# Performance work log

Measured on AMD Instinct MI355X. Metric: run time of the kernel, lower is better.

## Reference

```python
import jax, jax.numpy as jnp
import numpy as np

NUM_HEADS = 16
HIDDEN = 1024
HEAD_DIM = HIDDEN // NUM_HEADS
B, S, D = 2, 2048, 1024


def setup_inputs() -> dict:
    key = jax.random.key(0)
    ks = jax.random.split(key, 7)
    scale = 1.0 / np.sqrt(D)
    return {
        "query": jax.random.normal(ks[0], (B, S, D), dtype=jnp.float32),
        "key": jax.random.normal(ks[1], (B, S, D), dtype=jnp.float32),
        "value": jax.random.normal(ks[2], (B, S, D), dtype=jnp.float32),
        "Wk_w": jax.random.normal(ks[3], (HIDDEN, D), dtype=jnp.float32) * scale,
        "Wk_b": jax.random.normal(ks[4], (HIDDEN,), dtype=jnp.float32) * scale,
        "Wv_w": jax.random.normal(ks[5], (HIDDEN, D), dtype=jnp.float32) * scale,
        "Wv_b": jax.random.normal(ks[6], (HIDDEN,), dtype=jnp.float32) * scale,
    }


def reference(query, key, value, Wk_w, Wk_b, Wv_w, Wv_b):
    # NOTE: in the original torch module, self.W_v is assigned twice, so the
    # SAME Linear (Wv) projects both key and value; Wk projects query.
    b, s, _ = query.shape

    def split_heads(x):  # [b,s,hidden] -> [b,h,s,hd]
        return x.reshape(b, s, NUM_HEADS, HEAD_DIM).transpose(0, 2, 1, 3)

    q = split_heads(query @ Wk_w.T + Wk_b)
    k = split_heads(key @ Wv_w.T + Wv_b)
    v = split_heads(value @ Wv_w.T + Wv_b)

    scores = jnp.einsum("bhqd,bhkd->bhqk", q, k) / jnp.sqrt(
        jnp.asarray(HEAD_DIM, dtype=q.dtype))
    probs = jax.nn.softmax(scores, axis=-1)
    out = jnp.einsum("bhqk,bhkd->bhqd", probs, v)
    return out.transpose(0, 2, 1, 3).reshape(b, s, NUM_HEADS * HEAD_DIM)
```

## Files before the change

kernel.cpp:

```cpp
#include <hip/hip_runtime.h>
#include <stdint.h>

typedef unsigned short u16;
typedef uint32_t u32;
typedef __bf16 bf16x8 __attribute__((ext_vector_type(8)));
typedef float f32x4 __attribute__((ext_vector_type(4)));
typedef u16 u16x4 __attribute__((ext_vector_type(4)));
typedef u16 u16x8 __attribute__((ext_vector_type(8)));

#define XQ_OFF 0ul
#define XK_OFF 4194304ul
#define XV_OFF 8388608ul
#define WK_OFF 12582912ul
#define WV_OFF 13631488ul
#define Q_OFF  14680064ul
#define K_OFF  18874368ul
#define V_OFF  23068672ul

#define SCQ 0.18033688011112042f

#if __has_builtin(__builtin_amdgcn_exp2f)
#define EXP2F(x) __builtin_amdgcn_exp2f(x)
#else
#define EXP2F(x) exp2f(x)
#endif

__device__ __forceinline__ u16 f2bf(float f) {
  u32 u = __float_as_uint(f);
  u32 r = (u + 0x7fffu + ((u >> 16) & 1u)) >> 16;
  return (u16)r;
}

__device__ __forceinline__ u32 pk2(float a, float b) {
  typedef __bf16 bf2_t __attribute__((ext_vector_type(2)));
  typedef float f2_t __attribute__((ext_vector_type(2)));
  f2_t v; v[0] = a; v[1] = b;
  bf2_t h = __builtin_convertvector(v, bf2_t);
  union { bf2_t h; u32 u; } cv; cv.h = h; return cv.u;
}

__device__ __forceinline__ void load_lds16(const void* g, void* l) {
  __builtin_amdgcn_global_load_lds(
      (const __attribute__((address_space(1))) u32*)g,
      (__attribute__((address_space(3))) u32*)l, 16, 0, 0);
}

__global__ __launch_bounds__(256) void cvt_tile_kernel(
    const float* __restrict__ xq, const float* __restrict__ xk,
    const float* __restrict__ xv, const float* __restrict__ wk,
    const float* __restrict__ wv, u16* __restrict__ ws) {
  __shared__ u16 tile[4096];
  const int bid = blockIdx.x;
  const float* src; size_t dstbase; int rt, ktp;
  if (bid < 3072) {
    int m = bid >> 10, loc = bid & 1023;
    src = (m == 0) ? xq : (m == 1) ? xk : xv;
    dstbase = (size_t)m * 4194304ul;
    rt = loc >> 4; ktp = loc & 15;
  } else {
    int r2 = bid - 3072;
    int m = r2 >> 8, loc = r2 & 255;
    src = m ? wv : wk;
    dstbase = WK_OFF + (size_t)m * 1048576ul;
    rt = loc >> 4; ktp = loc & 15;
  }
  const int t = threadIdx.x;
  const int row0 = t >> 4, c = t & 15;
  const int k = c * 4;
  const float* s = src + (size_t)(rt * 64 + row0) * 1024ul + ktp * 64 + k;
#pragma unroll
  for (int i = 0; i < 4; ++i) {
    float4 v = *(const float4*)(s + (size_t)i * 16384ul);
    int row = row0 + i * 16;
    u32* p = (u32*)(tile + ((k >> 5) * 2048 + ((k >> 3) & 3) * 512 + row * 8 + (k & 7)));
    p[0] = pk2(v.x, v.y);
    p[1] = pk2(v.z, v.w);
  }
  __syncthreads();
  u16* dst = ws + dstbase + (size_t)(rt * 32 + ktp * 2) * 2048ul;
#pragma unroll
  for (int so = 0; so < 4096; so += 2048)
    *(u16x8*)(dst + so + t * 8) = *(const u16x8*)(tile + so + t * 8);
}

__global__ __launch_bounds__(256) void proj_kernel(u16* __restrict__ ws,
                                                   const float* __restrict__ bk,
                                                   const float* __restrict__ bv) {
  const int proj = blockIdx.z;
  const int mtile = blockIdx.x;
  const int ntile = blockIdx.y;
  const u16* A = ws + (size_t)proj * 4194304ul;
  const u16* Bw = ws + ((proj == 0) ? WK_OFF : WV_OFF);
  const float* bias = (proj == 0) ? bk : bv;
  u16* outQ = ws + Q_OFF;
  u16* outK = ws + K_OFF;
  u16* outV = ws + V_OFF;

  const int t = threadIdx.x;
  const int w = t >> 6, lane = t & 63, g = lane >> 4, c = lane & 15;
  const int wm = w >> 1, wn = w & 1;

  const u16* Aw = A + (size_t)(2 * mtile + wm) * 65536ul + (size_t)g * 512ul + (size_t)c * 8ul;
  const u16* Bb = Bw + (size_t)(2 * ntile + wn) * 65536ul + (size_t)g * 512ul + (size_t)c * 8ul;

  f32x4 acc[4][4];
#pragma unroll
  for (int mt = 0; mt < 4; ++mt)
#pragma unroll
    for (int nt = 0; nt < 4; ++nt) acc[mt][nt] = (f32x4){0.f, 0.f, 0.f, 0.f};

  bf16x8 a0[4], b0[4], a1[4], b1[4];
#pragma unroll
  for (int mt = 0; mt < 4; ++mt) {
    a0[mt] = *(const bf16x8*)(Aw + (size_t)(mt * 16) * 8ul);
    b0[mt] = *(const bf16x8*)(Bb + (size_t)(mt * 16) * 8ul);
  }

#pragma unroll 1
  for (int kk = 0; kk < 32; kk += 2) {
    const u16* An1 = Aw + (size_t)(kk + 1) * 2048ul;
    const u16* Bn1 = Bb + (size_t)(kk + 1) * 2048ul;
#pragma unroll
    for (int mt = 0; mt < 4; ++mt) {
      a1[mt] = *(const bf16x8*)(An1 + (size_t)(mt * 16) * 8ul);
      b1[mt] = *(const bf16x8*)(Bn1 + (size_t)(mt * 16) * 8ul);
    }
#pragma unroll
    for (int mt = 0; mt < 4; ++mt)
#pragma unroll
      for (int nt = 0; nt < 4; ++nt)
        acc[mt][nt] = __builtin_amdgcn_mfma_f32_16x16x32_bf16(a0[mt], b0[nt], acc[mt][nt], 0, 0, 0);
    if (kk + 2 < 32) {
      const u16* An2 = Aw + (size_t)(kk + 2) * 2048ul;
      const u16* Bn2 = Bb + (size_t)(kk + 2) * 2048ul;
#pragma unroll
      for (int mt = 0; mt < 4; ++mt) {
        a0[mt] = *(const bf16x8*)(An2 + (size_t)(mt * 16) * 8ul);
        b0[mt] = *(const bf16x8*)(Bn2 + (size_t)(mt * 16) * 8ul);
      }
    }
#pragma unroll
    for (int mt = 0; mt < 4; ++mt)
#pragma unroll
      for (int nt = 0; nt < 4; ++nt)
        acc[mt][nt] = __builtin_amdgcn_mfma_f32_16x16x32_bf16(a1[mt], b1[nt], acc[mt][nt], 0, 0, 0);
  }

  const int m0 = mtile * 128 + wm * 64, n0 = ntile * 128 + wn * 64;
#pragma unroll
  for (int nt = 0; nt < 4; ++nt) {
    const int col = n0 + nt * 16 + c;
    const float bvv = bias[col];
    const int h = col >> 6, d = col & 63;
#pragma unroll
    for (int mt = 0; mt < 4; ++mt) {
      const int mbase = m0 + mt * 16 + g * 4;
      const int b = mbase >> 11;
      const int bh = b * 16 + h;
      if (proj == 2) {
        const int s = mbase & 2047;
        u16x4 pk;
#pragma unroll
        for (int r = 0; r < 4; ++r) pk[r] = f2bf(acc[mt][nt][r] + bvv);
        size_t idx = (size_t)bh * 131072ul + (size_t)(s >> 6) * 4096ul +
                     (size_t)((s & 63) >> 3) * 512ul + (size_t)d * 8ul + (size_t)(s & 7);
        *(u16x4*)(outV + idx) = pk;
      } else {
        u16* dst = (proj == 0) ? outQ : outK;
#pragma unroll
        for (int r = 0; r < 4; ++r) {
          const int m = mbase + r;
          const int s = m & 2047;
          float y = acc[mt][nt][r] + bvv;
          if (proj == 0) y *= SCQ;
          size_t idx;
          if (proj == 0)
            idx = (size_t)bh * 131072ul + (size_t)(s >> 7) * 8192ul + (size_t)(d >> 3) * 1024ul +
                  (size_t)(s & 127) * 8ul + (size_t)(d & 7);
          else
            idx = (size_t)bh * 131072ul + (size_t)(s >> 6) * 4096ul + (size_t)(d >> 3) * 512ul +
                  (size_t)(s & 63) * 8ul + (size_t)(d & 7);
          dst[idx] = f2bf(y);
        }
      }
    }
  }
}

__global__ __launch_bounds__(256, 2) void attn_kernel(const u16* __restrict__ ws,
                                                      float* __restrict__ out) {
  const int bh = blockIdx.x, qtile = blockIdx.y;
  const int b = bh >> 4, h = bh & 15;
  const int t = threadIdx.x, w = t >> 6, lane = t & 63, g = lane >> 4, c = lane & 15;

  __shared__ u16 Ks[2][4096];
  __shared__ u16 Vs[2][4096];
  __shared__ __align__(16) u16 Ps[4][1280];

  const u16* Qg = ws + Q_OFF + (size_t)bh * 131072ul + (size_t)qtile * 8192ul;
  const u16* Kg = ws + K_OFF + (size_t)bh * 131072ul;
  const u16* Vg = ws + V_OFF + (size_t)bh * 131072ul;

  const int off = t * 16;
  load_lds16((const char*)Kg + off, (char*)Ks[0] + off);
  load_lds16((const char*)Kg + 4096 + off, (char*)Ks[0] + 4096 + off);
  load_lds16((const char*)Vg + off, (char*)Vs[0] + off);
  load_lds16((const char*)Vg + 4096 + off, (char*)Vs[0] + 4096 + off);

  bf16x8 qf[2][2];
#pragma unroll
  for (int ntq = 0; ntq < 2; ++ntq)
#pragma unroll
    for (int ks = 0; ks < 2; ++ks)
      qf[ntq][ks] = *(const bf16x8*)(Qg + (ks * 4 + g) * 1024 + (w * 32 + ntq * 16 + c) * 8);

  u16x8 ou;
#pragma unroll
  for (int i = 0; i < 8; ++i) ou[i] = (u16)0x3F80;
  union { u16x8 u; bf16x8 b; } ocv; ocv.u = ou;
  const bf16x8 onesf = ocv.b;

  f32x4 O[2][4], Lacc[2];
#pragma unroll
  for (int mtq = 0; mtq < 2; ++mtq) {
    Lacc[mtq] = (f32x4){0.f, 0.f, 0.f, 0.f};
#pragma unroll
    for (int nt = 0; nt < 4; ++nt) O[mtq][nt] = (f32x4){0.f, 0.f, 0.f, 0.f};
  }

  u16* Psw = Ps[w];
  __syncthreads();

#pragma unroll 1
  for (int j = 0; j < 32; ++j) {
    const int cur = j & 1;
    if (j < 31) {
      const char* Kn = (const char*)(Kg + (size_t)(j + 1) * 4096ul);
      const char* Vn = (const char*)(Vg + (size_t)(j + 1) * 4096ul);
      char* Kd = (char*)Ks[cur ^ 1];
      char* Vd = (char*)Vs[cur ^ 1];
      load_lds16(Kn + off, Kd + off);
      load_lds16(Kn + 4096 + off, Kd + 4096 + off);
      load_lds16(Vn + off, Vd + off);
      load_lds16(Vn + 4096 + off, Vd + 4096 + off);
    }
    const u16* Kc = Ks[cur];
    const u16* Vc = Vs[cur];

    f32x4 St[4][2];
#pragma unroll
    for (int mtk = 0; mtk < 4; ++mtk)
#pragma unroll
      for (int ntq = 0; ntq < 2; ++ntq) St[mtk][ntq] = (f32x4){0.f, 0.f, 0.f, 0.f};
#pragma unroll
    for (int ks = 0; ks < 2; ++ks) {
      bf16x8 kf[4];
#pragma unroll
      for (int mtk = 0; mtk < 4; ++mtk)
        kf[mtk] = *(const bf16x8*)(Kc + (ks * 4 + g) * 512 + (mtk * 16 + c) * 8);
#pragma unroll
      for (int mtk = 0; mtk < 4; ++mtk)
#pragma unroll
        for (int ntq = 0; ntq < 2; ++ntq)
          St[mtk][ntq] =
              __builtin_amdgcn_mfma_f32_16x16x32_bf16(kf[mtk], qf[ntq][ks], St[mtk][ntq], 0, 0, 0);
    }
#pragma unroll
    for (int mtk = 0; mtk < 4; ++mtk)
#pragma unroll
      for (int ntq = 0; ntq < 2; ++ntq)
#pragma unroll
        for (int r = 0; r < 4; ++r) St[mtk][ntq][r] = EXP2F(St[mtk][ntq][r]);
#pragma unroll
    for (int ksh = 0; ksh < 2; ++ksh) {
#pragma unroll
      for (int ntq = 0; ntq < 2; ++ntq)
#pragma unroll
        for (int m2 = 0; m2 < 2; ++m2) {
          const int mtk = ksh * 2 + m2;
          u32 lo = pk2(St[mtk][ntq][0], St[mtk][ntq][1]);
          u32 hi = pk2(St[mtk][ntq][2], St[mtk][ntq][3]);
          u32* p = (u32*)(Psw + (ntq * 16 + c) * 40 + m2 * 16 + g * 4);
          p[0] = lo; p[1] = hi;
        }
      asm volatile("s_waitcnt lgkmcnt(0)" ::: "memory");
      bf16x8 pf[2], vf[4];
#pragma unroll
      for (int mtq = 0; mtq < 2; ++mtq)
        pf[mtq] = *(const bf16x8*)(Psw + (mtq * 16 + c) * 40 + g * 8);
#pragma unroll
      for (int nt = 0; nt < 4; ++nt)
        vf[nt] = *(const bf16x8*)(Vc + (ksh * 4 + g) * 512 + (nt * 16 + c) * 8);
#pragma unroll
      for (int mtq = 0; mtq < 2; ++mtq) {
        Lacc[mtq] = __builtin_amdgcn_mfma_f32_16x16x32_bf16(pf[mtq], onesf, Lacc[mtq], 0, 0, 0);
#pragma unroll
        for (int nt = 0; nt < 4; ++nt)
          O[mtq][nt] = __builtin_amdgcn_mfma_f32_16x16x32_bf16(pf[mtq], vf[nt], O[mtq][nt], 0, 0, 0);
      }
    }
    __syncthreads();
  }

  const int q0 = qtile * 128 + w * 32;
#pragma unroll
  for (int mtq = 0; mtq < 2; ++mtq)
#pragma unroll
    for (int r = 0; r < 4; ++r) {
      const float inv = 1.0f / Lacc[mtq][r];
      const int q = q0 + mtq * 16 + g * 4 + r;
      float* rowp = out + (size_t)(b * 2048 + q) * 1024ul + h * 64;
#pragma unroll
      for (int nt = 0; nt < 4; ++nt) rowp[nt * 16 + c] = O[mtq][nt][r] * inv;
    }
}

extern "C" void kernel_launch(void* const* d_in, const int* in_sizes, int n_in,
                              void* d_out, int out_size, void* d_ws, size_t ws_size,
                              hipStream_t stream) {
  const float* q = (const float*)d_in[0];
  const float* k = (const float*)d_in[1];
  const float* v = (const float*)d_in[2];
  const float* wk = (const float*)d_in[3];
  const float* bk = (const float*)d_in[4];
  const float* wv = (const float*)d_in[5];
  const float* bv = (const float*)d_in[6];
  u16* ws = (u16*)d_ws;
  float* out = (float*)d_out;

  cvt_tile_kernel<<<3584, 256, 0, stream>>>(q, k, v, wk, wv, ws);
  proj_kernel<<<dim3(32, 8, 3), 256, 0, stream>>>(ws, bk, bv);
  attn_kernel<<<dim3(32, 16), 256, 0, stream>>>(ws, out);
}
```

Measured before the change: 192.8 us.

## Use 32x32 MFMA in projection and double attention waves per block

```diff
diff --git a/kernel.cpp b/kernel.cpp
--- a/kernel.cpp
+++ b/kernel.cpp
@@ -5,6 +5,7 @@
 typedef uint32_t u32;
 typedef __bf16 bf16x8 __attribute__((ext_vector_type(8)));
 typedef float f32x4 __attribute__((ext_vector_type(4)));
+typedef float f32x16 __attribute__((ext_vector_type(16)));
 typedef u16 u16x4 __attribute__((ext_vector_type(4)));
 typedef u16 u16x8 __attribute__((ext_vector_type(8)));
 
@@ -83,9 +84,9 @@
     *(u16x8*)(dst + so + t * 8) = *(const u16x8*)(tile + so + t * 8);
 }
 
-__global__ __launch_bounds__(256) void proj_kernel(u16* __restrict__ ws,
-                                                   const float* __restrict__ bk,
-                                                   const float* __restrict__ bv) {
+__global__ __launch_bounds__(256, 3) void proj_kernel(u16* __restrict__ ws,
+                                                      const float* __restrict__ bk,
+                                                      const float* __restrict__ bv) {
   const int proj = blockIdx.z;
   const int mtile = blockIdx.x;
   const int ntile = blockIdx.y;
@@ -97,97 +98,102 @@
   u16* outV = ws + V_OFF;
 
   const int t = threadIdx.x;
-  const int w = t >> 6, lane = t & 63, g = lane >> 4, c = lane & 15;
+  const int w = t >> 6, lane = t & 63;
   const int wm = w >> 1, wn = w & 1;
-
-  const u16* Aw = A + (size_t)(2 * mtile + wm) * 65536ul + (size_t)g * 512ul + (size_t)c * 8ul;
-  const u16* Bb = Bw + (size_t)(2 * ntile + wn) * 65536ul + (size_t)g * 512ul + (size_t)c * 8ul;
-
-  f32x4 acc[4][4];
-#pragma unroll
-  for (int mt = 0; mt < 4; ++mt)
-#pragma unroll
-    for (int nt = 0; nt < 4; ++nt) acc[mt][nt] = (f32x4){0.f, 0.f, 0.f, 0.f};
-
-  bf16x8 a0[4], b0[4], a1[4], b1[4];
-#pragma unroll
-  for (int mt = 0; mt < 4; ++mt) {
-    a0[mt] = *(const bf16x8*)(Aw + (size_t)(mt * 16) * 8ul);
-    b0[mt] = *(const bf16x8*)(Bb + (size_t)(mt * 16) * 8ul);
-  }
+  const int c32 = lane & 31, g2 = lane >> 5;
+
+  const u16* Aw = A + (size_t)(2 * mtile + wm) * 65536ul + (size_t)g2 * 512ul + (size_t)c32 * 8ul;
+  const u16* Bb = Bw + (size_t)(2 * ntile + wn) * 65536ul + (size_t)g2 * 512ul + (size_t)c32 * 8ul;
+
+  f32x16 acc[2][2];
+#pragma unroll
+  for (int rf = 0; rf < 2; ++rf)
+#pragma unroll
+    for (int cf = 0; cf < 2; ++cf)
+#pragma unroll
+      for (int i = 0; i < 16; ++i) acc[rf][cf][i] = 0.f;
+
+  bf16x8 ab[4][2], bb[4][2];
+#pragma unroll
+  for (int s = 0; s < 4; ++s)
+#pragma unroll
+    for (int f = 0; f < 2; ++f) {
+      ab[s][f] = *(const bf16x8*)(Aw + (size_t)s * 1024ul + f * 256);
+      bb[s][f] = *(const bf16x8*)(Bb + (size_t)s * 1024ul + f * 256);
+    }
 
 #pragma unroll 1
-  for (int kk = 0; kk < 32; kk += 2) {
-    const u16* An1 = Aw + (size_t)(kk + 1) * 2048ul;
-    const u16* Bn1 = Bb + (size_t)(kk + 1) * 2048ul;
-#pragma unroll
-    for (int mt = 0; mt < 4; ++mt) {
-      a1[mt] = *(const bf16x8*)(An1 + (size_t)(mt * 16) * 8ul);
-      b1[mt] = *(const bf16x8*)(Bn1 + (size_t)(mt * 16) * 8ul);
-    }
-#pragma unroll
-    for (int mt = 0; mt < 4; ++mt)
-#pragma unroll
-      for (int nt = 0; nt < 4; ++nt)
-        acc[mt][nt] = __builtin_amdgcn_mfma_f32_16x16x32_bf16(a0[mt], b0[nt], acc[mt][nt], 0, 0, 0);
-    if (kk + 2 < 32) {
-      const u16* An2 = Aw + (size_t)(kk + 2) * 2048ul;
-      const u16* Bn2 = Bb + (size_t)(kk + 2) * 2048ul;
-#pragma unroll
-      for (int mt = 0; mt < 4; ++mt) {
-        a0[mt] = *(const bf16x8*)(An2 + (size_t)(mt * 16) * 8ul);
-        b0[mt] = *(const bf16x8*)(Bn2 + (size_t)(mt * 16) * 8ul);
+  for (int ks = 0; ks < 60; ks += 4) {
+#pragma unroll
+    for (int s = 0; s < 4; ++s) {
+#pragma unroll
+      for (int rf = 0; rf < 2; ++rf)
+#pragma unroll
+        for (int cf = 0; cf < 2; ++cf)
+          acc[rf][cf] =
+              __builtin_amdgcn_mfma_f32_32x32x16_bf16(ab[s][rf], bb[s][cf], acc[rf][cf], 0, 0, 0);
+      const size_t o = (size_t)(ks + 4 + s) * 1024ul;
+#pragma unroll
+      for (int f = 0; f < 2; ++f) {
+        ab[s][f] = *(const bf16x8*)(Aw + o + f * 256);
+        bb[s][f] = *(const bf16x8*)(Bb + o + f * 256);
       }
     }
-#pragma unroll
-    for (int mt = 0; mt < 4; ++mt)
-#pragma unroll
-      for (int nt = 0; nt < 4; ++nt)
-        acc[mt][nt] = __builtin_amdgcn_mfma_f32_16x16x32_bf16(a1[mt], b1[nt], acc[mt][nt], 0, 0, 0);
-  }
-
-  const int m0 = mtile * 128 + wm * 64, n0 = ntile * 128 + wn * 64;
-#pragma unroll
-  for (int nt = 0; nt < 4; ++nt) {
-    const int col = n0 + nt * 16 + c;
+  }
+#pragma unroll
+  for (int s = 0; s < 4; ++s)
+#pragma unroll
+    for (int rf = 0; rf < 2; ++rf)
+#pragma unroll
+      for (int cf = 0; cf < 2; ++cf)
+        acc[rf][cf] =
+            __builtin_amdgcn_mfma_f32_32x32x16_bf16(ab[s][rf], bb[s][cf], acc[rf][cf], 0, 0, 0);
+
+  const int m0w = mtile * 128 + wm * 64, n0w = ntile * 128 + wn * 64;
+#pragma unroll
+  for (int cf = 0; cf < 2; ++cf) {
+    const int col = n0w + cf * 32 + c32;
     const float bvv = bias[col];
     const int h = col >> 6, d = col & 63;
 #pragma unroll
-    for (int mt = 0; mt < 4; ++mt) {
-      const int mbase = m0 + mt * 16 + g * 4;
-      const int b = mbase >> 11;
-      const int bh = b * 16 + h;
-      if (proj == 2) {
-        const int s = mbase & 2047;
-        u16x4 pk;
-#pragma unroll
-        for (int r = 0; r < 4; ++r) pk[r] = f2bf(acc[mt][nt][r] + bvv);
-        size_t idx = (size_t)bh * 131072ul + (size_t)(s >> 6) * 4096ul +
-                     (size_t)((s & 63) >> 3) * 512ul + (size_t)d * 8ul + (size_t)(s & 7);
-        *(u16x4*)(outV + idx) = pk;
-      } else {
-        u16* dst = (proj == 0) ? outQ : outK;
-#pragma unroll
-        for (int r = 0; r < 4; ++r) {
-          const int m = mbase + r;
-          const int s = m & 2047;
-          float y = acc[mt][nt][r] + bvv;
-          if (proj == 0) y *= SCQ;
-          size_t idx;
-          if (proj == 0)
-            idx = (size_t)bh * 131072ul + (size_t)(s >> 7) * 8192ul + (size_t)(d >> 3) * 1024ul +
-                  (size_t)(s & 127) * 8ul + (size_t)(d & 7);
-          else
-            idx = (size_t)bh * 131072ul + (size_t)(s >> 6) * 4096ul + (size_t)(d >> 3) * 512ul +
-                  (size_t)(s & 63) * 8ul + (size_t)(d & 7);
-          dst[idx] = f2bf(y);
+    for (int rf = 0; rf < 2; ++rf) {
+#pragma unroll
+      for (int q = 0; q < 4; ++q) {
+        const int mbase = m0w + rf * 32 + q * 8 + g2 * 4;
+        const int b = mbase >> 11;
+        const int bh = b * 16 + h;
+        if (proj == 2) {
+          const int s = mbase & 2047;
+          u16x4 pk;
+#pragma unroll
+          for (int r = 0; r < 4; ++r) pk[r] = f2bf(acc[rf][cf][q * 4 + r] + bvv);
+          size_t idx = (size_t)bh * 131072ul + (size_t)(s >> 6) * 4096ul +
+                       (size_t)((s & 63) >> 3) * 512ul + (size_t)d * 8ul + (size_t)(s & 7);
+          *(u16x4*)(outV + idx) = pk;
+        } else {
+          u16* dst = (proj == 0) ? outQ : outK;
+#pragma unroll
+          for (int r = 0; r < 4; ++r) {
+            const int m = mbase + r;
+            const int s = m & 2047;
+            float y = acc[rf][cf][q * 4 + r] + bvv;
+            if (proj == 0) y *= SCQ;
+            size_t idx;
+            if (proj == 0)
+              idx = (size_t)bh * 131072ul + (size_t)(s >> 7) * 8192ul + (size_t)(d >> 3) * 1024ul +
+                    (size_t)(s & 127) * 8ul + (size_t)(d & 7);
+            else
+              idx = (size_t)bh * 131072ul + (size_t)(s >> 6) * 4096ul + (size_t)(d >> 3) * 512ul +
+                    (size_t)(s & 63) * 8ul + (size_t)(d & 7);
+            dst[idx] = f2bf(y);
+          }
         }
       }
     }
   }
 }
 
-__global__ __launch_bounds__(256, 2) void attn_kernel(const u16* __restrict__ ws,
+__global__ __launch_bounds__(512, 4) void attn_kernel(const u16* __restrict__ ws,
                                                       float* __restrict__ out) {
   const int bh = blockIdx.x, qtile = blockIdx.y;
   const int b = bh >> 4, h = bh & 15;
@@ -195,7 +201,7 @@
 
   __shared__ u16 Ks[2][4096];
   __shared__ u16 Vs[2][4096];
-  __shared__ __align__(16) u16 Ps[4][1280];
+  __shared__ __align__(16) u16 Ps[8][640];
 
   const u16* Qg = ws + Q_OFF + (size_t)bh * 131072ul + (size_t)qtile * 8192ul;
   const u16* Kg = ws + K_OFF + (size_t)bh * 131072ul;
@@ -203,16 +209,12 @@
 
   const int off = t * 16;
   load_lds16((const char*)Kg + off, (char*)Ks[0] + off);
-  load_lds16((const char*)Kg + 4096 + off, (char*)Ks[0] + 4096 + off);
   load_lds16((const char*)Vg + off, (char*)Vs[0] + off);
-  load_lds16((const char*)Vg + 4096 + off, (char*)Vs[0] + 4096 + off);
-
-  bf16x8 qf[2][2];
-#pragma unroll
-  for (int ntq = 0; ntq < 2; ++ntq)
-#pragma unroll
-    for (int ks = 0; ks < 2; ++ks)
-      qf[ntq][ks] = *(const bf16x8*)(Qg + (ks * 4 + g) * 1024 + (w * 32 + ntq * 16 + c) * 8);
+
+  bf16x8 qf[2];
+#pragma unroll
+  for (int ks = 0; ks < 2; ++ks)
+    qf[ks] = *(const bf16x8*)(Qg + (ks * 4 + g) * 1024 + (w * 16 + c) * 8);
 
   u16x8 ou;
 #pragma unroll
@@ -220,13 +222,10 @@
   union { u16x8 u; bf16x8 b; } ocv; ocv.u = ou;
   const bf16x8 onesf = ocv.b;
 
-  f32x4 O[2][4], Lacc[2];
-#pragma unroll
-  for (int mtq = 0; mtq < 2; ++mtq) {
-    Lacc[mtq] = (f32x4){0.f, 0.f, 0.f, 0.f};
-#pragma unroll
-    for (int nt = 0; nt < 4; ++nt) O[mtq][nt] = (f32x4){0.f, 0.f, 0.f, 0.f};
-  }
+  f32x4 O[4], Lacc;
+  Lacc = (f32x4){0.f, 0.f, 0.f, 0.f};
+#pragma unroll
+  for (int nt = 0; nt < 4; ++nt) O[nt] = (f32x4){0.f, 0.f, 0.f, 0.f};
 
   u16* Psw = Ps[w];
   __syncthreads();
@@ -237,21 +236,15 @@
     if (j < 31) {
       const char* Kn = (const char*)(Kg + (size_t)(j + 1) * 4096ul);
       const char* Vn = (const char*)(Vg + (size_t)(j + 1) * 4096ul);
-      char* Kd = (char*)Ks[cur ^ 1];
-      char* Vd = (char*)Vs[cur ^ 1];
-      load_lds16(Kn + off, Kd + off);
-      load_lds16(Kn + 4096 + off, Kd + 4096 + off);
-      load_lds16(Vn + off, Vd + off);
-      load_lds16(Vn + 4096 + off, Vd + 4096 + off);
+      load_lds16(Kn + off, (char*)Ks[cur ^ 1] + off);
+      load_lds16(Vn + off, (char*)Vs[cur ^ 1] + off);
     }
     const u16* Kc = Ks[cur];
     const u16* Vc = Vs[cur];
 
-    f32x4 St[4][2];
-#pragma unroll
-    for (int mtk = 0; mtk < 4; ++mtk)
-#pragma unroll
-      for (int ntq = 0; ntq < 2; ++ntq) St[mtk][ntq] = (f32x4){0.f, 0.f, 0.f, 0.f};
+    f32x4 St[4];
+#pragma unroll
+    for (int mtk = 0; mtk < 4; ++mtk) St[mtk] = (f32x4){0.f, 0.f, 0.f, 0.f};
 #pragma unroll
     for (int ks = 0; ks < 2; ++ks) {
       bf16x8 kf[4];
@@ -260,59 +253,45 @@
         kf[mtk] = *(const bf16x8*)(Kc + (ks * 4 + g) * 512 + (mtk * 16 + c) * 8);
 #pragma unroll
       for (int mtk = 0; mtk < 4; ++mtk)
-#pragma unroll
-        for (int ntq = 0; ntq < 2; ++ntq)
-          St[mtk][ntq] =
-              __builtin_amdgcn_mfma_f32_16x16x32_bf16(kf[mtk], qf[ntq][ks], St[mtk][ntq], 0, 0, 0);
+        St[mtk] = __builtin_amdgcn_mfma_f32_16x16x32_bf16(kf[mtk], qf[ks], St[mtk], 0, 0, 0);
     }
 #pragma unroll
     for (int mtk = 0; mtk < 4; ++mtk)
 #pragma unroll
-      for (int ntq = 0; ntq < 2; ++ntq)
-#pragma unroll
-        for (int r = 0; r < 4; ++r) St[mtk][ntq][r] = EXP2F(St[mtk][ntq][r]);
+      for (int r = 0; r < 4; ++r) St[mtk][r] = EXP2F(St[mtk][r]);
 #pragma unroll
     for (int ksh = 0; ksh < 2; ++ksh) {
 #pragma unroll
-      for (int ntq = 0; ntq < 2; ++ntq)
-#pragma unroll
-        for (int m2 = 0; m2 < 2; ++m2) {
-          const int mtk = ksh * 2 + m2;
-          u32 lo = pk2(St[mtk][ntq][0], St[mtk][ntq][1]);
-          u32 hi = pk2(St[mtk][ntq][2], St[mtk][ntq][3]);
-          u32* p = (u32*)(Psw + (ntq * 16 + c) * 40 + m2 * 16 + g * 4);
-          p[0] = lo; p[1] = hi;
-        }
+      for (int m2 = 0; m2 < 2; ++m2) {
+        const int mtk = ksh * 2 + m2;
+        u32 lo = pk2(St[mtk][0], St[mtk][1]);
+        u32 hi = pk2(St[mtk][2], St[mtk][3]);
+        u32* p = (u32*)(Psw + c * 40 + m2 * 16 + g * 4);
+        p[0] = lo; p[1] = hi;
+      }
       asm volatile("s_waitcnt lgkmcnt(0)" ::: "memory");
-      bf16x8 pf[2], vf[4];
-#pragma unroll
-      for (int mtq = 0; mtq < 2; ++mtq)
-        pf[mtq] = *(const bf16x8*)(Psw + (mtq * 16 + c) * 40 + g * 8);
+      bf16x8 pf, vf[4];
+      pf = *(const bf16x8*)(Psw + c * 40 + g * 8);
 #pragma unroll
       for (int nt = 0; nt < 4; ++nt)
         vf[nt] = *(const bf16x8*)(Vc + (ksh * 4 + g) * 512 + (nt * 16 + c) * 8);
-#pragma unroll
-      for (int mtq = 0; mtq < 2; ++mtq) {
-        Lacc[mtq] = __builtin_amdgcn_mfma_f32_16x16x32_bf16(pf[mtq], onesf, Lacc[mtq], 0, 0, 0);
-#pragma unroll
-        for (int nt = 0; nt < 4; ++nt)
-          O[mtq][nt] = __builtin_amdgcn_mfma_f32_16x16x32_bf16(pf[mtq], vf[nt], O[mtq][nt], 0, 0, 0);
-      }
+      Lacc = __builtin_amdgcn_mfma_f32_16x16x32_bf16(pf, onesf, Lacc, 0, 0, 0);
+#pragma unroll
+      for (int nt = 0; nt < 4; ++nt)
+        O[nt] = __builtin_amdgcn_mfma_f32_16x16x32_bf16(pf, vf[nt], O[nt], 0, 0, 0);
     }
     __syncthreads();
   }
 
-  const int q0 = qtile * 128 + w * 32;
-#pragma unroll
-  for (int mtq = 0; mtq < 2; ++mtq)
-#pragma unroll
-    for (int r = 0; r < 4; ++r) {
-      const float inv = 1.0f / Lacc[mtq][r];
-      const int q = q0 + mtq * 16 + g * 4 + r;
-      float* rowp = out + (size_t)(b * 2048 + q) * 1024ul + h * 64;
-#pragma unroll
-      for (int nt = 0; nt < 4; ++nt) rowp[nt * 16 + c] = O[mtq][nt][r] * inv;
-    }
+  const int q0 = qtile * 128 + w * 16;
+#pragma unroll
+  for (int r = 0; r < 4; ++r) {
+    const float inv = 1.0f / Lacc[r];
+    const int q = q0 + g * 4 + r;
+    float* rowp = out + (size_t)(b * 2048 + q) * 1024ul + h * 64;
+#pragma unroll
+    for (int nt = 0; nt < 4; ++nt) rowp[nt * 16 + c] = O[nt][r] * inv;
+  }
 }
 
 extern "C" void kernel_launch(void* const* d_in, const int* in_sizes, int n_in,
@@ -330,5 +309,5 @@
 
   cvt_tile_kernel<<<3584, 256, 0, stream>>>(q, k, v, wk, wv, ws);
   proj_kernel<<<dim3(32, 8, 3), 256, 0, stream>>>(ws, bk, bv);
-  attn_kernel<<<dim3(32, 16), 256, 0, stream>>>(ws, out);
-}
+  attn_kernel<<<dim3(32, 16), 512, 0, stream>>>(ws, out);
+}
```

After: 184.8 us. 4.1% less time.
